# Kernel optimization log

Hardware: AMD Instinct MI355X
Metric: run time of the kernel (lower is better)

The kernel has to match this reference:

```python
import jax, jax.numpy as jnp
import numpy as np

B, L = 4, 1024
D_IN, D_MODEL = 2, 512
N_LAYERS, D_STATE, D_CONV, EXPAND, DT_RANK = 2, 16, 4, 2, 32
D_INNER = EXPAND * D_MODEL
EPS = 1e-5


def setup_inputs() -> dict:
    key = jax.random.key(0)
    ks = jax.random.split(key, 10)
    s = 0.02
    return {
        "x": jax.random.normal(ks[0], (B, L, D_IN), jnp.float32),
        "emb_W": jax.random.normal(ks[1], (D_MODEL, D_IN), jnp.float32) * s,
        "emb_b": jnp.zeros((D_MODEL,), jnp.float32),
        "norm_w": jnp.ones((N_LAYERS, D_MODEL), jnp.float32),
        "in_proj_W": jax.random.normal(ks[2], (N_LAYERS, 2 * D_INNER, D_MODEL), jnp.float32) * s,
        "conv_W": jax.random.normal(ks[3], (N_LAYERS, D_INNER, 1, D_CONV), jnp.float32) * s,
        "conv_b": jnp.zeros((N_LAYERS, D_INNER), jnp.float32),
        "x_proj_W": jax.random.normal(ks[4], (N_LAYERS, DT_RANK + 2 * D_STATE, D_INNER), jnp.float32) * s,
        "dt_proj_W": jax.random.normal(ks[5], (N_LAYERS, D_INNER, DT_RANK), jnp.float32) * s,
        "dt_proj_b": jax.random.uniform(ks[6], (N_LAYERS, D_INNER), jnp.float32, -4.0, -2.0),
        "A_log": jnp.log(jnp.broadcast_to(jnp.arange(1, D_STATE + 1, dtype=jnp.float32), (N_LAYERS, D_INNER, D_STATE)) + 0.0),
        "Dskip": jnp.ones((N_LAYERS, D_INNER), jnp.float32),
        "out_proj_W": jax.random.normal(ks[7], (N_LAYERS, D_MODEL, D_INNER), jnp.float32) * s,
        "normf_w": jnp.ones((D_MODEL,), jnp.float32),
    }


def rmsnorm(x, w):
    return x * jax.lax.rsqrt(jnp.mean(x * x, axis=-1, keepdims=True) + EPS) * w


def selective_scan(u, delta, A, Bm, Cm, Dskip):
    # u, delta: (B,L,ED); A: (ED,N); Bm, Cm: (B,L,N); Dskip: (ED,)
    deltaA = jnp.exp(delta[..., None] * A)                      # (B,L,ED,N)
    BX = (delta[..., None] * Bm[:, :, None, :]) * u[..., None]  # (B,L,ED,N)

    def step(h, inp):
        dA, bx, c = inp
        h = dA * h + bx                       # (B,ED,N)
        y = jnp.einsum('ben,bn->be', h, c)    # (B,ED)
        return h, y

    h0 = jnp.zeros((u.shape[0], u.shape[2], A.shape[1]), u.dtype)
    _, ys = jax.lax.scan(step, h0, (deltaA.swapaxes(0, 1), BX.swapaxes(0, 1), Cm.swapaxes(0, 1)))
    y = ys.swapaxes(0, 1)                     # (B,L,ED)
    return y + Dskip * u


def mamba_layer(x, norm_w, ipW, cW, cb, xpW, dtW, dtb, A_log, Dk, opW):
    h = rmsnorm(x, norm_w)
    xz = h @ ipW.T                            # (B,L,2*ED)
    u, z = jnp.split(xz, 2, axis=-1)
    # causal depthwise conv over sequence dim
    uc = jax.lax.conv_general_dilated(
        u.swapaxes(1, 2), cW, window_strides=(1,), padding=[(D_CONV - 1, 0)],
        feature_group_count=D_INNER, dimension_numbers=('NCH', 'OIH', 'NCH'))
    u = jax.nn.silu(uc.swapaxes(1, 2) + cb)   # (B,L,ED)
    xdb = u @ xpW.T                           # (B,L,dt_rank+2N)
    dt, Bm, Cm = jnp.split(xdb, [DT_RANK, DT_RANK + D_STATE], axis=-1)
    delta = jax.nn.softplus(dt @ dtW.T + dtb)
    A = -jnp.exp(A_log)
    y = selective_scan(u, delta, A, Bm, Cm, Dk)
    y = y * jax.nn.silu(z)
    return x + y @ opW.T


def reference(x, emb_W, emb_b, norm_w, in_proj_W, conv_W, conv_b, x_proj_W,
              dt_proj_W, dt_proj_b, A_log, Dskip, out_proj_W, normf_w):
    h = x @ emb_W.T + emb_b                   # (B,L,D_MODEL)
    for l in range(N_LAYERS):
        h = mamba_layer(h, norm_w[l], in_proj_W[l], conv_W[l], conv_b[l],
                        x_proj_W[l], dt_proj_W[l], dt_proj_b[l], A_log[l],
                        Dskip[l], out_proj_W[l])
    return rmsnorm(h, normf_w)
```

## Files before the change

### kernel.cpp

```cpp
#include <hip/hip_runtime.h>
#include <math.h>
#include <stddef.h>

#define BB 4
#define LL 1024
#define DM 512
#define ED 1024
#define NST 16
#define DTR 32
#define XDBC 64
#define BL (BB*LL)
#define CS 16
#define NC 64
#define XKS 16
#define XPAD 68

typedef __attribute__((ext_vector_type(8))) short bf16x8;
typedef __attribute__((ext_vector_type(4))) float f32x4;
typedef unsigned short ushort_t;

__device__ __forceinline__ float silu_f(float x) { return x / (1.f + __expf(-x)); }

__device__ __forceinline__ ushort_t f2b(float f) {
    unsigned int u = __float_as_uint(f);
    unsigned int r = (u + 0x7FFFu + ((u >> 16) & 1u)) >> 16;
    return (ushort_t)r;
}
__device__ __forceinline__ float b2f(ushort_t v) {
    return __uint_as_float(((unsigned int)v) << 16);
}

__device__ __forceinline__ void gload16(const ushort_t* g, ushort_t* l) {
    __builtin_amdgcn_global_load_lds(
        (const __attribute__((address_space(1))) unsigned int*)g,
        (__attribute__((address_space(3))) unsigned int*)l, 16, 0, 0);
}

__global__ void k_init(const float* __restrict__ x, const float* __restrict__ embW,
                       const float* __restrict__ embB, float* __restrict__ h,
                       const float* __restrict__ ipW, const float* __restrict__ opW,
                       ushort_t* __restrict__ wip, ushort_t* __restrict__ wop,
                       int nEmb, int n1, int n2) {
    int i = blockIdx.x * 256 + threadIdx.x;
    if (i < nEmb) {
        int d = i % DM, r = i / DM;
        h[i] = x[r * 2 + 0] * embW[d * 2 + 0] + x[r * 2 + 1] * embW[d * 2 + 1] + embB[d];
        return;
    }
    i -= nEmb;
    const float* src; ushort_t* dst; int q;
    if (i < n1) { src = ipW; dst = wip; q = i; }
    else if (i < n1 + n2) { src = opW; dst = wop; q = i - n1; }
    else return;
    float4 v = *(const float4*)(src + (size_t)q * 4);
    ushort_t o[4] = {f2b(v.x), f2b(v.y), f2b(v.z), f2b(v.w)};
    *(uint2*)(dst + (size_t)q * 4) = *(uint2*)o;
}

template <int BF16OUT>
__global__ __launch_bounds__(256) void k_rmsnorm(const float* __restrict__ in,
                                                 const float* __restrict__ w,
                                                 void* __restrict__ outp) {
    int m = blockIdx.x;
    int tid = threadIdx.x;
    const float* row = in + (size_t)m * DM;
    float2 v = *(const float2*)(row + tid * 2);
    float ss = v.x * v.x + v.y * v.y;
    #pragma unroll
    for (int o = 32; o > 0; o >>= 1) ss += __shfl_down(ss, o, 64);
    __shared__ float red[4];
    int wid = tid >> 6;
    if ((tid & 63) == 0) red[wid] = ss;
    __syncthreads();
    float tot = red[0] + red[1] + red[2] + red[3];
    float rs = rsqrtf(tot * (1.f / DM) + 1e-5f);
    float2 wv = *(const float2*)(w + tid * 2);
    float ox = v.x * rs * wv.x;
    float oy = v.y * rs * wv.y;
    if (BF16OUT) {
        ushort_t o[2] = {f2b(ox), f2b(oy)};
        *(unsigned int*)((ushort_t*)outp + (size_t)m * DM + tid * 2) = *(unsigned int*)o;
    } else {
        *(float2*)((float*)outp + (size_t)m * DM + tid * 2) = make_float2(ox, oy);
    }
}

template <int ADDRES, int BF16OUT, int NT>
__global__ __launch_bounds__(256) void k_bgemm(const ushort_t* __restrict__ A,
                                               const ushort_t* __restrict__ W,
                                               const float* __restrict__ Res,
                                               void* __restrict__ C,
                                               int M, int N, int K, int lda, int ldc) {
    __shared__ ushort_t As[128 * 32];
    __shared__ ushort_t Bs[NT * 32];
    constexpr int NFJ = NT / 32;
    int tid = threadIdx.x;
    int bm = blockIdx.y * 128, bn = blockIdx.x * NT;
    int wave = tid >> 6, lane = tid & 63;
    int wr = wave >> 1, wc = wave & 1;
    int lr = lane & 15;
    int kc = lane >> 4;
    f32x4 acc[4][NFJ];
    #pragma unroll
    for (int i = 0; i < 4; ++i)
        #pragma unroll
        for (int j = 0; j < NFJ; ++j) acc[i][j] = (f32x4){0.f, 0.f, 0.f, 0.f};

    for (int k0 = 0; k0 < K; k0 += 32) {
        __syncthreads();
        #pragma unroll
        for (int ii = 0; ii < 2; ++ii) {
            int g = wave * 128 + ii * 64 + lane;
            int row = g >> 2;
            int c = (g & 3) ^ ((g >> 3) & 3);
            gload16(A + (size_t)(bm + row) * lda + k0 + c * 8,
                    As + (size_t)(wave * 128 + ii * 64) * 8);
        }
        #pragma unroll
        for (int ii = 0; ii < NFJ / 2; ++ii) {
            int g = wave * (NFJ / 2) * 64 + ii * 64 + lane;
            int row = g >> 2;
            int c = (g & 3) ^ ((g >> 3) & 3);
            gload16(W + (size_t)(bn + row) * K + k0 + c * 8,
                    Bs + (size_t)(wave * (NFJ / 2) * 64 + ii * 64) * 8);
        }
        __syncthreads();
        bf16x8 af[4], bfr[NFJ];
        #pragma unroll
        for (int i = 0; i < 4; ++i) {
            int ra = wr * 64 + i * 16 + lr;
            int ca = kc ^ ((ra >> 1) & 3);
            af[i] = *(const bf16x8*)(As + ra * 32 + ca * 8);
        }
        #pragma unroll
        for (int j = 0; j < NFJ; ++j) {
            int rb = wc * (NT / 2) + j * 16 + lr;
            int cb = kc ^ ((rb >> 1) & 3);
            bfr[j] = *(const bf16x8*)(Bs + rb * 32 + cb * 8);
        }
        #pragma unroll
        for (int i = 0; i < 4; ++i)
            #pragma unroll
            for (int j = 0; j < NFJ; ++j)
                acc[i][j] = __builtin_amdgcn_mfma_f32_16x16x32_bf16(af[i], bfr[j], acc[i][j], 0, 0, 0);
    }
    int crow0 = bm + wr * 64 + (lane >> 4) * 4;
    #pragma unroll
    for (int i = 0; i < 4; ++i)
        #pragma unroll
        for (int j = 0; j < NFJ; ++j)
            #pragma unroll
            for (int r = 0; r < 4; ++r) {
                size_t off = (size_t)(crow0 + i * 16 + r) * ldc + bn + wc * (NT / 2) + j * 16 + lr;
                float v = acc[i][j][r];
                if (ADDRES) v += Res[off];
                if (BF16OUT) ((ushort_t*)C)[off] = f2b(v);
                else         ((float*)C)[off] = v;
            }
}

__global__ __launch_bounds__(256) void k_cxp(const ushort_t* __restrict__ xzb,
                                             const float* __restrict__ cw,
                                             const float* __restrict__ cb,
                                             const float* __restrict__ xpW,
                                             ushort_t* __restrict__ ub,
                                             float* __restrict__ Pp) {
    __shared__ float As[64][XPAD];
    __shared__ float Ws[64][XPAD];
    int tid = threadIdx.x;
    int ks = blockIdx.x;
    int bm = blockIdx.y * 64;
    int ec0 = ks * 64;

    {
        int r0 = (tid >> 4) * 4;
        int e4 = (tid & 15) * 4;
        int e = ec0 + e4;
        float cw4[4][4], cb4[4];
        #pragma unroll
        for (int j = 0; j < 4; ++j) {
            float4 w = *(const float4*)(cw + (size_t)(e + j) * 4);
            cw4[j][0] = w.x; cw4[j][1] = w.y; cw4[j][2] = w.z; cw4[j][3] = w.w;
        }
        float4 cbv = *(const float4*)(cb + e);
        cb4[0] = cbv.x; cb4[1] = cbv.y; cb4[2] = cbv.z; cb4[3] = cbv.w;
        #pragma unroll
        for (int i = 0; i < 4; ++i) {
            int row = bm + r0 + i;
            int tloc = row & (LL - 1);
            const ushort_t* xrow = xzb + (size_t)row * 2048 + e;
            uint2 z2 = make_uint2(0, 0);
            uint2 v3 = *(const uint2*)xrow;
            uint2 v2 = (tloc >= 1) ? *(const uint2*)(xrow - 2048) : z2;
            uint2 v1 = (tloc >= 2) ? *(const uint2*)(xrow - 4096) : z2;
            uint2 v0 = (tloc >= 3) ? *(const uint2*)(xrow - 6144) : z2;
            const ushort_t* p0 = (const ushort_t*)&v0;
            const ushort_t* p1 = (const ushort_t*)&v1;
            const ushort_t* p2 = (const ushort_t*)&v2;
            const ushort_t* p3 = (const ushort_t*)&v3;
            ushort_t ures[4];
            #pragma unroll
            for (int j = 0; j < 4; ++j) {
                float a = cb4[j] + b2f(p0[j]) * cw4[j][0] + b2f(p1[j]) * cw4[j][1]
                                 + b2f(p2[j]) * cw4[j][2] + b2f(p3[j]) * cw4[j][3];
                float uu = silu_f(a);
                As[e4 + j][r0 + i] = uu;
                ures[j] = f2b(uu);
            }
            *(uint2*)(ub + (size_t)row * ED + e) = *(uint2*)ures;
        }
    }
    {
        int r = tid >> 2;
        int kc = (tid & 3) * 16;
        const float4* wp = (const float4*)(xpW + (size_t)r * ED + ec0 + kc);
        #pragma unroll
        for (int i = 0; i < 4; ++i) {
            float4 wv = wp[i];
            Ws[kc + i * 4 + 0][r] = wv.x; Ws[kc + i * 4 + 1][r] = wv.y;
            Ws[kc + i * 4 + 2][r] = wv.z; Ws[kc + i * 4 + 3][r] = wv.w;
        }
    }
    __syncthreads();
    int tm = (tid >> 4) * 4;
    int tn = (tid & 15) * 4;
    float acc[4][4] = {};
    #pragma unroll 4
    for (int k = 0; k < 64; ++k) {
        float4 a = *(const float4*)&As[k][tm];
        float4 b = *(const float4*)&Ws[k][tn];
        acc[0][0] += a.x * b.x; acc[0][1] += a.x * b.y; acc[0][2] += a.x * b.z; acc[0][3] += a.x * b.w;
        acc[1][0] += a.y * b.x; acc[1][1] += a.y * b.y; acc[1][2] += a.y * b.z; acc[1][3] += a.y * b.w;
        acc[2][0] += a.z * b.x; acc[2][1] += a.z * b.y; acc[2][2] += a.z * b.z; acc[2][3] += a.z * b.w;
        acc[3][0] += a.w * b.x; acc[3][1] += a.w * b.y; acc[3][2] += a.w * b.z; acc[3][3] += a.w * b.w;
    }
    float* pp = Pp + (size_t)ks * BL * XDBC;
    #pragma unroll
    for (int i = 0; i < 4; ++i)
        *(float4*)(pp + (size_t)(bm + tm + i) * XDBC + tn) =
            make_float4(acc[i][0], acc[i][1], acc[i][2], acc[i][3]);
}

__global__ void k_xred(const float* __restrict__ Pp, float* __restrict__ xdb) {
    int i = blockIdx.x * 256 + threadIdx.x;
    float4 s = make_float4(0.f, 0.f, 0.f, 0.f);
    #pragma unroll
    for (int sl = 0; sl < XKS; ++sl) {
        float4 v = *(const float4*)(Pp + (size_t)sl * BL * XDBC + (size_t)i * 4);
        s.x += v.x; s.y += v.y; s.z += v.z; s.w += v.w;
    }
    *(float4*)(xdb + (size_t)i * 4) = s;
}

__global__ __launch_bounds__(256) void k_scan1(const float* __restrict__ xdb,
                                               const ushort_t* __restrict__ u,
                                               const float* __restrict__ dtW,
                                               const float* __restrict__ dtb,
                                               const float* __restrict__ A_log,
                                               ushort_t* __restrict__ P,
                                               float* __restrict__ S) {
    __shared__ float Xs[CS][XDBC];
    int tid = threadIdx.x;
    int e = ((blockIdx.x & 3) << 8) + tid;
    int c = (blockIdx.x >> 2) & (NC - 1);
    int b = blockIdx.x >> 8;
    size_t r0 = (size_t)b * LL + c * CS;
    {
        int t = tid >> 4, q = (tid & 15) * 4;
        *(float4*)&Xs[t][q] = *(const float4*)(xdb + (r0 + t) * XDBC + q);
    }
    float Ac[16];
    const float4* ap = (const float4*)(A_log + (size_t)e * NST);
    #pragma unroll
    for (int q = 0; q < 4; ++q) {
        float4 a = ap[q];
        Ac[q * 4 + 0] = -__expf(a.x); Ac[q * 4 + 1] = -__expf(a.y);
        Ac[q * 4 + 2] = -__expf(a.z); Ac[q * 4 + 3] = -__expf(a.w);
    }
    float dtw[32];
    const float4* wq = (const float4*)(dtW + (size_t)e * DTR);
    #pragma unroll
    for (int q = 0; q < 8; ++q) {
        float4 w = wq[q];
        dtw[q * 4 + 0] = w.x; dtw[q * 4 + 1] = w.y;
        dtw[q * 4 + 2] = w.z; dtw[q * 4 + 3] = w.w;
    }
    float bias = dtb[e];
    __syncthreads();
    float dv[CS];
    #pragma unroll
    for (int t = 0; t < CS; ++t) {
        float acc = bias;
        #pragma unroll
        for (int q = 0; q < 8; ++q) {
            float4 d = *(const float4*)&Xs[t][q * 4];
            acc += d.x * dtw[q * 4 + 0] + d.y * dtw[q * 4 + 1] +
                   d.z * dtw[q * 4 + 2] + d.w * dtw[q * 4 + 3];
        }
        dv[t] = (acc > 20.f) ? acc : __logf(1.f + __expf(acc));
    }
    float h[16] = {};
    float s = 0.f;
    const ushort_t* up = u + r0 * ED + e;
    for (int tt = 0; tt < CS; ++tt) {
        float d = dv[tt];
        float uv = b2f(up[(size_t)tt * ED]);
        s += d;
        float du = d * uv;
        const float4* bp = (const float4*)&Xs[tt][DTR];
        #pragma unroll
        for (int q = 0; q < 4; ++q) {
            float4 bv = bp[q];
            h[q * 4 + 0] = __expf(d * Ac[q * 4 + 0]) * h[q * 4 + 0] + du * bv.x;
            h[q * 4 + 1] = __expf(d * Ac[q * 4 + 1]) * h[q * 4 + 1] + du * bv.y;
            h[q * 4 + 2] = __expf(d * Ac[q * 4 + 2]) * h[q * 4 + 2] + du * bv.z;
            h[q * 4 + 3] = __expf(d * Ac[q * 4 + 3]) * h[q * 4 + 3] + du * bv.w;
        }
    }
    ushort_t pb[16];
    #pragma unroll
    for (int n = 0; n < 16; ++n) pb[n] = f2b(h[n]);
    uint4* pp = (uint4*)(P + ((size_t)(b * NC + c) * ED + e) * NST);
    pp[0] = ((uint4*)pb)[0];
    pp[1] = ((uint4*)pb)[1];
    S[(size_t)(b * NC + c) * ED + e] = s;
}

__global__ __launch_bounds__(256) void k_scan2(ushort_t* __restrict__ P,
                                               const float* __restrict__ S,
                                               const float* __restrict__ A_log) {
    int i = blockIdx.x * 256 + threadIdx.x;
    int n = i & 15;
    int e = (i >> 4) & (ED - 1);
    int b = i >> 14;
    float Ac = -__expf(A_log[(size_t)e * NST + n]);
    float hin = 0.f;
    for (int c = 0; c < NC; ++c) {
        size_t base = (size_t)(b * NC + c) * ED + e;
        float p = b2f(P[base * NST + n]);
        float s = S[base];
        P[base * NST + n] = f2b(hin);
        hin = __expf(Ac * s) * hin + p;
    }
}

__global__ __launch_bounds__(256) void k_scan3(const float* __restrict__ xdb,
                                               const ushort_t* __restrict__ u,
                                               const ushort_t* __restrict__ xzb,
                                               const float* __restrict__ dtW,
                                               const float* __restrict__ dtb,
                                               const float* __restrict__ A_log,
                                               const float* __restrict__ Dskip,
                                               const ushort_t* __restrict__ P,
                                               ushort_t* __restrict__ yb) {
    __shared__ float Xs[CS][XDBC];
    int tid = threadIdx.x;
    int e = ((blockIdx.x & 3) << 8) + tid;
    int c = (blockIdx.x >> 2) & (NC - 1);
    int b = blockIdx.x >> 8;
    size_t r0 = (size_t)b * LL + c * CS;
    {
        int t = tid >> 4, q = (tid & 15) * 4;
        *(float4*)&Xs[t][q] = *(const float4*)(xdb + (r0 + t) * XDBC + q);
    }
    float Ac[16];
    const float4* ap = (const float4*)(A_log + (size_t)e * NST);
    #pragma unroll
    for (int q = 0; q < 4; ++q) {
        float4 a = ap[q];
        Ac[q * 4 + 0] = -__expf(a.x); Ac[q * 4 + 1] = -__expf(a.y);
        Ac[q * 4 + 2] = -__expf(a.z); Ac[q * 4 + 3] = -__expf(a.w);
    }
    float dtw[32];
    const float4* wq = (const float4*)(dtW + (size_t)e * DTR);
    #pragma unroll
    for (int q = 0; q < 8; ++q) {
        float4 w = wq[q];
        dtw[q * 4 + 0] = w.x; dtw[q * 4 + 1] = w.y;
        dtw[q * 4 + 2] = w.z; dtw[q * 4 + 3] = w.w;
    }
    float bias = dtb[e];
    __syncthreads();
    float dv[CS];
    #pragma unroll
    for (int t = 0; t < CS; ++t) {
        float acc = bias;
        #pragma unroll
        for (int q = 0; q < 8; ++q) {
            float4 d = *(const float4*)&Xs[t][q * 4];
            acc += d.x * dtw[q * 4 + 0] + d.y * dtw[q * 4 + 1] +
                   d.z * dtw[q * 4 + 2] + d.w * dtw[q * 4 + 3];
        }
        dv[t] = (acc > 20.f) ? acc : __logf(1.f + __expf(acc));
    }
    float h[16];
    const uint4* pp4 = (const uint4*)(P + ((size_t)(b * NC + c) * ED + e) * NST);
    uint4 pA = pp4[0], pB = pp4[1];
    const ushort_t* pw0 = (const ushort_t*)&pA;
    const ushort_t* pw1 = (const ushort_t*)&pB;
    #pragma unroll
    for (int n = 0; n < 8; ++n) { h[n] = b2f(pw0[n]); h[8 + n] = b2f(pw1[n]); }
    float Dk = Dskip[e];
    const ushort_t* up = u + r0 * ED + e;
    const ushort_t* zp = xzb + r0 * 2048 + 1024 + e;
    ushort_t* yp = yb + r0 * ED + e;
    for (int tt = 0; tt < CS; ++tt) {
        float d = dv[tt];
        float uv = b2f(up[(size_t)tt * ED]);
        float zv = b2f(zp[(size_t)tt * 2048]);
        float du = d * uv;
        const float4* bp = (const float4*)&Xs[tt][DTR];
        const float4* cp = (const float4*)&Xs[tt][DTR + NST];
        float y = 0.f;
        #pragma unroll
        for (int q = 0; q < 4; ++q) {
            float4 bv = bp[q];
            float4 cv = cp[q];
            h[q * 4 + 0] = __expf(d * Ac[q * 4 + 0]) * h[q * 4 + 0] + du * bv.x;
            h[q * 4 + 1] = __expf(d * Ac[q * 4 + 1]) * h[q * 4 + 1] + du * bv.y;
            h[q * 4 + 2] = __expf(d * Ac[q * 4 + 2]) * h[q * 4 + 2] + du * bv.z;
            h[q * 4 + 3] = __expf(d * Ac[q * 4 + 3]) * h[q * 4 + 3] + du * bv.w;
            y += h[q * 4 + 0] * cv.x + h[q * 4 + 1] * cv.y +
                 h[q * 4 + 2] * cv.z + h[q * 4 + 3] * cv.w;
        }
        yp[(size_t)tt * ED] = f2b((y + Dk * uv) * silu_f(zv));
    }
}

extern "C" void kernel_launch(void* const* d_in, const int* in_sizes, int n_in,
                              void* d_out, int out_size, void* d_ws, size_t ws_size,
                              hipStream_t stream) {
    const float* x     = (const float*)d_in[0];
    const float* embW  = (const float*)d_in[1];
    const float* embB  = (const float*)d_in[2];
    const float* normw = (const float*)d_in[3];
    const float* ipW   = (const float*)d_in[4];
    const float* cW    = (const float*)d_in[5];
    const float* cb    = (const float*)d_in[6];
    const float* xpW   = (const float*)d_in[7];
    const float* dtW   = (const float*)d_in[8];
    const float* dtb   = (const float*)d_in[9];
    const float* Alog  = (const float*)d_in[10];
    const float* Dsk   = (const float*)d_in[11];
    const float* opW   = (const float*)d_in[12];
    const float* normfw= (const float*)d_in[13];
    float* out = (float*)d_out;

    float* ws  = (float*)d_ws;
    float* h   = ws;
    ushort_t* xzb = (ushort_t*)(h + (size_t)BL * DM);
    ushort_t* ub  = xzb + (size_t)BL * 2 * ED;
    float* xdb = (float*)(ub + (size_t)BL * ED);
    float* Pp  = xdb + (size_t)BL * XDBC;
    float* S   = Pp + (size_t)XKS * BL * XDBC;
    ushort_t* wip = (ushort_t*)(S + (size_t)BB * NC * ED);
    ushort_t* wop = wip + (size_t)2 * 2 * ED * DM;
    ushort_t* yb  = wop + (size_t)2 * DM * ED;
    ushort_t* P   = (ushort_t*)Pp;
    ushort_t* hnb = (ushort_t*)d_out;

    int nEmb = BL * DM;
    int n1 = 2 * 2 * ED * DM / 4, n2 = 2 * DM * ED / 4;
    k_init<<<(nEmb + n1 + n2 + 255) / 256, 256, 0, stream>>>(
        x, embW, embB, h, ipW, opW, wip, wop, nEmb, n1, n2);

    for (int l = 0; l < 2; ++l) {
        const float* Al = Alog + (size_t)l * ED * NST;
        const float* dtWl = dtW + (size_t)l * ED * DTR;
        const float* dtbl = dtb + (size_t)l * ED;
        k_rmsnorm<1><<<BL, 256, 0, stream>>>(h, normw + (size_t)l * DM, hnb);
        k_bgemm<0, 1, 128><<<dim3(2 * ED / 128, BL / 128), 256, 0, stream>>>(
            hnb, wip + (size_t)l * 2 * ED * DM, nullptr, xzb, BL, 2 * ED, DM, DM, 2 * ED);
        k_cxp<<<dim3(XKS, BL / 64), 256, 0, stream>>>(
            xzb, cW + (size_t)l * ED * 4, cb + (size_t)l * ED,
            xpW + (size_t)l * XDBC * ED, ub, Pp);
        k_xred<<<BL * XDBC / 4 / 256, 256, 0, stream>>>(Pp, xdb);
        k_scan1<<<BB * NC * (ED / 256), 256, 0, stream>>>(
            xdb, ub, dtWl, dtbl, Al, P, S);
        k_scan2<<<BB * ED * NST / 256, 256, 0, stream>>>(P, S, Al);
        k_scan3<<<BB * NC * (ED / 256), 256, 0, stream>>>(
            xdb, ub, xzb, dtWl, dtbl, Al, Dsk + (size_t)l * ED, P, yb);
        k_bgemm<1, 0, 64><<<dim3(DM / 64, BL / 128), 256, 0, stream>>>(
            yb, wop + (size_t)l * DM * ED, h, h, BL, DM, ED, ED, DM);
    }
    k_rmsnorm<0><<<BL, 256, 0, stream>>>(h, normfw, out);
}
```

Baseline: 274.4 us.

## Replace split-K reduction with atomics, cache delta in fp16, halve scan chunk

```diff
diff --git a/kernel.cpp b/kernel.cpp
--- a/kernel.cpp
+++ b/kernel.cpp
@@ -10,8 +10,8 @@
 #define DTR 32
 #define XDBC 64
 #define BL (BB*LL)
-#define CS 16
-#define NC 64
+#define CS 8
+#define NC 128
 #define XKS 16
 #define XPAD 68
 
@@ -28,6 +28,14 @@
 }
 __device__ __forceinline__ float b2f(ushort_t v) {
     return __uint_as_float(((unsigned int)v) << 16);
+}
+__device__ __forceinline__ ushort_t f2h(float f) {
+    _Float16 h = (_Float16)f;
+    return *(ushort_t*)&h;
+}
+__device__ __forceinline__ float h2f(ushort_t v) {
+    _Float16 h = *(_Float16*)&v;
+    return (float)h;
 }
 
 __device__ __forceinline__ void gload16(const ushort_t* g, ushort_t* l) {
@@ -60,9 +68,14 @@
 template <int BF16OUT>
 __global__ __launch_bounds__(256) void k_rmsnorm(const float* __restrict__ in,
                                                  const float* __restrict__ w,
-                                                 void* __restrict__ outp) {
+                                                 void* __restrict__ outp,
+                                                 float* __restrict__ xdbz) {
     int m = blockIdx.x;
     int tid = threadIdx.x;
+    if (BF16OUT) {
+        if (tid < 16)
+            *(float4*)(xdbz + (size_t)m * XDBC + tid * 4) = make_float4(0.f, 0.f, 0.f, 0.f);
+    }
     const float* row = in + (size_t)m * DM;
     float2 v = *(const float2*)(row + tid * 2);
     float ss = v.x * v.x + v.y * v.y;
@@ -164,7 +177,7 @@
                                              const float* __restrict__ cb,
                                              const float* __restrict__ xpW,
                                              ushort_t* __restrict__ ub,
-                                             float* __restrict__ Pp) {
+                                             float* __restrict__ xdb) {
     __shared__ float As[64][XPAD];
     __shared__ float Ws[64][XPAD];
     int tid = threadIdx.x;
@@ -234,22 +247,11 @@
         acc[2][0] += a.z * b.x; acc[2][1] += a.z * b.y; acc[2][2] += a.z * b.z; acc[2][3] += a.z * b.w;
         acc[3][0] += a.w * b.x; acc[3][1] += a.w * b.y; acc[3][2] += a.w * b.z; acc[3][3] += a.w * b.w;
     }
-    float* pp = Pp + (size_t)ks * BL * XDBC;
     #pragma unroll
     for (int i = 0; i < 4; ++i)
-        *(float4*)(pp + (size_t)(bm + tm + i) * XDBC + tn) =
-            make_float4(acc[i][0], acc[i][1], acc[i][2], acc[i][3]);
-}
-
-__global__ void k_xred(const float* __restrict__ Pp, float* __restrict__ xdb) {
-    int i = blockIdx.x * 256 + threadIdx.x;
-    float4 s = make_float4(0.f, 0.f, 0.f, 0.f);
-    #pragma unroll
-    for (int sl = 0; sl < XKS; ++sl) {
-        float4 v = *(const float4*)(Pp + (size_t)sl * BL * XDBC + (size_t)i * 4);
-        s.x += v.x; s.y += v.y; s.z += v.z; s.w += v.w;
-    }
-    *(float4*)(xdb + (size_t)i * 4) = s;
+        #pragma unroll
+        for (int j = 0; j < 4; ++j)
+            atomicAdd(xdb + (size_t)(bm + tm + i) * XDBC + tn + j, acc[i][j]);
 }
 
 __global__ __launch_bounds__(256) void k_scan1(const float* __restrict__ xdb,
@@ -258,16 +260,17 @@
                                                const float* __restrict__ dtb,
                                                const float* __restrict__ A_log,
                                                ushort_t* __restrict__ P,
-                                               float* __restrict__ S) {
+                                               float* __restrict__ S,
+                                               ushort_t* __restrict__ dyh) {
     __shared__ float Xs[CS][XDBC];
     int tid = threadIdx.x;
     int e = ((blockIdx.x & 3) << 8) + tid;
     int c = (blockIdx.x >> 2) & (NC - 1);
-    int b = blockIdx.x >> 8;
+    int b = blockIdx.x >> 9;
     size_t r0 = (size_t)b * LL + c * CS;
     {
-        int t = tid >> 4, q = (tid & 15) * 4;
-        *(float4*)&Xs[t][q] = *(const float4*)(xdb + (r0 + t) * XDBC + q);
+        int t = tid >> 5, q = (tid & 31) * 2;
+        *(float2*)&Xs[t][q] = *(const float2*)(xdb + (r0 + t) * XDBC + q);
     }
     float Ac[16];
     const float4* ap = (const float4*)(A_log + (size_t)e * NST);
@@ -298,6 +301,7 @@
                    d.z * dtw[q * 4 + 2] + d.w * dtw[q * 4 + 3];
         }
         dv[t] = (acc > 20.f) ? acc : __logf(1.f + __expf(acc));
+        dyh[(r0 + t) * ED + e] = f2h(dv[t]);
     }
     float h[16] = {};
     float s = 0.f;
@@ -347,8 +351,7 @@
 __global__ __launch_bounds__(256) void k_scan3(const float* __restrict__ xdb,
                                                const ushort_t* __restrict__ u,
                                                const ushort_t* __restrict__ xzb,
-                                               const float* __restrict__ dtW,
-                                               const float* __restrict__ dtb,
+                                               const ushort_t* __restrict__ dyh,
                                                const float* __restrict__ A_log,
                                                const float* __restrict__ Dskip,
                                                const ushort_t* __restrict__ P,
@@ -357,11 +360,11 @@
     int tid = threadIdx.x;
     int e = ((blockIdx.x & 3) << 8) + tid;
     int c = (blockIdx.x >> 2) & (NC - 1);
-    int b = blockIdx.x >> 8;
+    int b = blockIdx.x >> 9;
     size_t r0 = (size_t)b * LL + c * CS;
     {
-        int t = tid >> 4, q = (tid & 15) * 4;
-        *(float4*)&Xs[t][q] = *(const float4*)(xdb + (r0 + t) * XDBC + q);
+        int t = tid >> 5, q = (tid & 31) * 2;
+        *(float2*)&Xs[t][q] = *(const float2*)(xdb + (r0 + t) * XDBC + q);
     }
     float Ac[16];
     const float4* ap = (const float4*)(A_log + (size_t)e * NST);
@@ -370,28 +373,6 @@
         float4 a = ap[q];
         Ac[q * 4 + 0] = -__expf(a.x); Ac[q * 4 + 1] = -__expf(a.y);
         Ac[q * 4 + 2] = -__expf(a.z); Ac[q * 4 + 3] = -__expf(a.w);
-    }
-    float dtw[32];
-    const float4* wq = (const float4*)(dtW + (size_t)e * DTR);
-    #pragma unroll
-    for (int q = 0; q < 8; ++q) {
-        float4 w = wq[q];
-        dtw[q * 4 + 0] = w.x; dtw[q * 4 + 1] = w.y;
-        dtw[q * 4 + 2] = w.z; dtw[q * 4 + 3] = w.w;
-    }
-    float bias = dtb[e];
-    __syncthreads();
-    float dv[CS];
-    #pragma unroll
-    for (int t = 0; t < CS; ++t) {
-        float acc = bias;
-        #pragma unroll
-        for (int q = 0; q < 8; ++q) {
-            float4 d = *(const float4*)&Xs[t][q * 4];
-            acc += d.x * dtw[q * 4 + 0] + d.y * dtw[q * 4 + 1] +
-                   d.z * dtw[q * 4 + 2] + d.w * dtw[q * 4 + 3];
-        }
-        dv[t] = (acc > 20.f) ? acc : __logf(1.f + __expf(acc));
     }
     float h[16];
     const uint4* pp4 = (const uint4*)(P + ((size_t)(b * NC + c) * ED + e) * NST);
@@ -401,11 +382,13 @@
     #pragma unroll
     for (int n = 0; n < 8; ++n) { h[n] = b2f(pw0[n]); h[8 + n] = b2f(pw1[n]); }
     float Dk = Dskip[e];
+    __syncthreads();
+    const ushort_t* dp = dyh + r0 * ED + e;
     const ushort_t* up = u + r0 * ED + e;
     const ushort_t* zp = xzb + r0 * 2048 + 1024 + e;
     ushort_t* yp = yb + r0 * ED + e;
     for (int tt = 0; tt < CS; ++tt) {
-        float d = dv[tt];
+        float d = h2f(dp[(size_t)tt * ED]);
         float uv = b2f(up[(size_t)tt * ED]);
         float zv = b2f(zp[(size_t)tt * 2048]);
         float du = d * uv;
@@ -451,13 +434,13 @@
     ushort_t* xzb = (ushort_t*)(h + (size_t)BL * DM);
     ushort_t* ub  = xzb + (size_t)BL * 2 * ED;
     float* xdb = (float*)(ub + (size_t)BL * ED);
-    float* Pp  = xdb + (size_t)BL * XDBC;
-    float* S   = Pp + (size_t)XKS * BL * XDBC;
+    ushort_t* P = (ushort_t*)(xdb + (size_t)BL * XDBC);
+    float* S   = (float*)(P + (size_t)BB * NC * ED * NST);
     ushort_t* wip = (ushort_t*)(S + (size_t)BB * NC * ED);
     ushort_t* wop = wip + (size_t)2 * 2 * ED * DM;
     ushort_t* yb  = wop + (size_t)2 * DM * ED;
-    ushort_t* P   = (ushort_t*)Pp;
     ushort_t* hnb = (ushort_t*)d_out;
+    ushort_t* dyh = (ushort_t*)d_out;
 
     int nEmb = BL * DM;
     int n1 = 2 * 2 * ED * DM / 4, n2 = 2 * DM * ED / 4;
@@ -468,20 +451,19 @@
         const float* Al = Alog + (size_t)l * ED * NST;
         const float* dtWl = dtW + (size_t)l * ED * DTR;
         const float* dtbl = dtb + (size_t)l * ED;
-        k_rmsnorm<1><<<BL, 256, 0, stream>>>(h, normw + (size_t)l * DM, hnb);
+        k_rmsnorm<1><<<BL, 256, 0, stream>>>(h, normw + (size_t)l * DM, hnb, xdb);
         k_bgemm<0, 1, 128><<<dim3(2 * ED / 128, BL / 128), 256, 0, stream>>>(
             hnb, wip + (size_t)l * 2 * ED * DM, nullptr, xzb, BL, 2 * ED, DM, DM, 2 * ED);
         k_cxp<<<dim3(XKS, BL / 64), 256, 0, stream>>>(
             xzb, cW + (size_t)l * ED * 4, cb + (size_t)l * ED,
-            xpW + (size_t)l * XDBC * ED, ub, Pp);
-        k_xred<<<BL * XDBC / 4 / 256, 256, 0, stream>>>(Pp, xdb);
+            xpW + (size_t)l * XDBC * ED, ub, xdb);
         k_scan1<<<BB * NC * (ED / 256), 256, 0, stream>>>(
-            xdb, ub, dtWl, dtbl, Al, P, S);
+            xdb, ub, dtWl, dtbl, Al, P, S, dyh);
         k_scan2<<<BB * ED * NST / 256, 256, 0, stream>>>(P, S, Al);
         k_scan3<<<BB * NC * (ED / 256), 256, 0, stream>>>(
-            xdb, ub, xzb, dtWl, dtbl, Al, Dsk + (size_t)l * ED, P, yb);
+            xdb, ub, xzb, dyh, Al, Dsk + (size_t)l * ED, P, yb);
         k_bgemm<1, 0, 64><<<dim3(DM / 64, BL / 128), 256, 0, stream>>>(
             yb, wop + (size_t)l * DM * ED, h, h, BL, DM, ED, ED, DM);
     }
-    k_rmsnorm<0><<<BL, 256, 0, stream>>>(h, normfw, out);
-}
+    k_rmsnorm<0><<<BL, 256, 0, stream>>>(h, normfw, out, nullptr);
+}
```

Measured after the change: 353.5 us. 1.29x slower.
